# Kernel optimization log

Measured on AMD Instinct MI355X. Metric: run time of the kernel, lower is better.

Reference implementation:

```python
import jax, jax.numpy as jnp
import numpy as np

LN_EPS = 1e-5

def _layernorm(x, gamma, beta):
    mu = jnp.mean(x, axis=-1, keepdims=True)
    var = jnp.mean((x - mu) ** 2, axis=-1, keepdims=True)
    return (x - mu) / jnp.sqrt(var + LN_EPS) * gamma + beta

def setup_inputs() -> dict:
    key = jax.random.key(0)
    ks = jax.random.split(key, 12)
    B, S, D, V, H = 2, 2048, 1024, 32000, 16
    d_ff = 4 * D
    inp = {}
    inp["V"] = jax.random.randint(ks[0], (B, S), 0, V, dtype=jnp.int64)
    inp["num_heads"] = H
    sc = 0.02
    inp["emb"] = jax.random.normal(ks[1], (V, D), dtype=jnp.float32) * sc
    inp["w_o"] = jax.random.normal(ks[2], (D, D), dtype=jnp.float32) * sc
    inp["w1"] = jax.random.normal(ks[3], (D, d_ff), dtype=jnp.float32) * sc
    inp["b1"] = jnp.zeros((d_ff,), dtype=jnp.float32)
    inp["w2"] = jax.random.normal(ks[4], (d_ff, D), dtype=jnp.float32) * sc
    inp["b2"] = jnp.zeros((D,), dtype=jnp.float32)
    inp["gamma1"] = jnp.ones((D,), dtype=jnp.float32)
    inp["beta1"] = jnp.zeros((D,), dtype=jnp.float32)
    inp["gamma2"] = jnp.ones((D,), dtype=jnp.float32)
    inp["beta2"] = jnp.zeros((D,), dtype=jnp.float32)
    return inp

def reference(V, num_heads, emb, w_o, w1, b1, w2, b2, gamma1, beta1, gamma2, beta2):
    # Embedding lookup: [B, S, D]
    x = emb[V]
    B, S, D = x.shape
    hd = D // num_heads
    # NOTE: the original forward never applies w_q/w_k/w_v -- q=k=v=embedding,
    # split per head along the feature dim.
    qh = x.reshape(B, S, num_heads, hd)
    scores = jnp.einsum("bqhd,bkhd->bhqk", qh, qh) / jnp.sqrt(jnp.float32(hd))
    attn = jax.nn.softmax(scores, axis=-1)
    ctx = jnp.einsum("bhqk,bkhd->bqhd", attn, qh).reshape(B, S, D)
    attn_out = ctx @ w_o
    x1 = _layernorm(x + attn_out, gamma1, beta1)
    ff = jax.nn.relu(x1 @ w1 + b1) @ w2 + b2
    return _layernorm(x1 + ff, gamma2, beta2)
```

## Files before the change

kernel.cpp:

```cpp
#include <hip/hip_runtime.h>
#include <hip/hip_bf16.h>

#define B_  2
#define S_  2048
#define D_  1024
#define H_  16
#define HD_ 64
#define DFF 4096
#define NT  (B_ * S_)

typedef __bf16 bf16;
typedef __bf16 bf16x8 __attribute__((ext_vector_type(8)));
typedef __bf16 bf16x4 __attribute__((ext_vector_type(4)));
typedef __bf16 bf16x2 __attribute__((ext_vector_type(2)));
typedef float  f32x4  __attribute__((ext_vector_type(4)));
typedef float  f32x16 __attribute__((ext_vector_type(16)));
typedef int    i32x2  __attribute__((ext_vector_type(2)));

typedef const __attribute__((address_space(1))) unsigned int GLB_U32;
typedef __attribute__((address_space(3))) unsigned int AS3_U32;

__device__ __forceinline__ void gload16(const void* g, void* l) {
    __builtin_amdgcn_global_load_lds((GLB_U32*)g, (AS3_U32*)l, 16, 0, 0);
}

#define MFMA32(A, B, C) __builtin_amdgcn_mfma_f32_32x32x16_bf16(A, B, C, 0, 0, 0)
#define MFMA16(A, B, C) __builtin_amdgcn_mfma_f32_16x16x32_bf16(A, B, C, 0, 0, 0)

__device__ __forceinline__ unsigned pk2(float a, float b) {
    union { bf16x2 v; unsigned u; } t;
    t.v[0] = (bf16)a; t.v[1] = (bf16)b;
    return t.u;
}

#define ATT_SCL 0.18033688011112042f

#define PREP_EMB  (B_ * (S_ / 32) * (D_ / 32))
#define PREP_WO   ((D_ / 32) * (D_ / 32))
#define PREP_W1   ((D_ / 32) * (DFF / 32))
#define PREP_W2   ((DFF / 32) * (D_ / 32))
#define PREP_TOT  (PREP_EMB + PREP_WO + PREP_W1 + PREP_W2)

__device__ __forceinline__ void transcvt_tile(const float* src, bf16* dst,
                                              int R, int C, int tile,
                                              float* tf, int tx, int ty) {
    int tiles_c = C >> 5;
    int r0 = (tile / tiles_c) << 5;
    int c0 = (tile % tiles_c) << 5;
#pragma unroll
    for (int i = 0; i < 4; i++)
        tf[(ty + i * 8) * 33 + tx] = src[(size_t)(r0 + ty + i * 8) * C + c0 + tx];
    __syncthreads();
#pragma unroll
    for (int i = 0; i < 4; i++)
        dst[(size_t)(c0 + ty + i * 8) * R + r0 + tx] = (bf16)tf[tx * 33 + ty + i * 8];
}

__global__ __launch_bounds__(256)
void k_prep(const int* __restrict__ V, const float* __restrict__ emb,
            bf16* __restrict__ xb, bf16* __restrict__ xT,
            const float* __restrict__ w_o, bf16* __restrict__ wobT,
            const float* __restrict__ w1, bf16* __restrict__ w1T,
            const float* __restrict__ w2, bf16* __restrict__ w2T) {
    __shared__ float tf[32 * 33];
    int bidx = blockIdx.x;
    int tx = threadIdx.x & 31, ty = threadIdx.x >> 5;

    if (bidx < PREP_EMB) {
        bf16* tb = (bf16*)tf;
        const int tiles_d = D_ / 32;
        int b   = bidx / ((S_ / 32) * tiles_d);
        int rem = bidx % ((S_ / 32) * tiles_d);
        int ts = rem / tiles_d, td = rem % tiles_d;
        int s0 = ts * 32, d0 = td * 32;
        bf16* xbb = xb + (size_t)b * S_ * D_;
        bf16* dst = xT + (size_t)b * D_ * S_;
#pragma unroll
        for (int i = 0; i < 4; i++) {
            int srow = s0 + ty + i * 8;
            int vid = V[b * S_ + srow];
            bf16 val = (bf16)emb[(size_t)vid * D_ + d0 + tx];
            xbb[(size_t)srow * D_ + d0 + tx] = val;
            tb[(ty + i * 8) * 34 + tx] = val;
        }
        __syncthreads();
#pragma unroll
        for (int i = 0; i < 4; i++)
            dst[(size_t)(d0 + ty + i * 8) * S_ + s0 + tx] = tb[tx * 34 + ty + i * 8];
    } else if (bidx < PREP_EMB + PREP_WO) {
        transcvt_tile(w_o, wobT, D_, D_, bidx - PREP_EMB, tf, tx, ty);
    } else if (bidx < PREP_EMB + PREP_WO + PREP_W1) {
        transcvt_tile(w1, w1T, D_, DFF, bidx - PREP_EMB - PREP_WO, tf, tx, ty);
    } else {
        transcvt_tile(w2, w2T, DFF, D_, bidx - PREP_EMB - PREP_WO - PREP_W1, tf, tx, ty);
    }
}

__global__ __launch_bounds__(256)
void k_attn(const bf16* __restrict__ xb, const bf16* __restrict__ xT,
            bf16* __restrict__ ctxb) {
    __shared__ alignas(16) bf16 Kt[3][64][64];
    __shared__ alignas(16) bf16 Vt[3][64][64];

    int bh = blockIdx.x >> 4;
    int qt = blockIdx.x & 15;
    int b = bh >> 4, h = bh & 15;
    int tid = threadIdx.x;
    int w = tid >> 6, lane = tid & 63;
    int l31 = lane & 31, hi = lane >> 5;

    const bf16* xq = xb + (size_t)b * S_ * D_ + h * HD_;
    const bf16* vT = xT + ((size_t)b * D_ + h * HD_) * S_;

    int q0 = qt * 128 + w * 32;

    bf16x8 qf[4];
#pragma unroll
    for (int c = 0; c < 4; c++) {
        qf[c] = *(const bf16x8*)(xq + (size_t)(q0 + l31) * D_ + c * 16 + hi * 8);
#pragma unroll
        for (int i = 0; i < 8; i++)
            qf[c][i] = (bf16)((float)qf[c][i] * ATT_SCL);
    }

    bf16x8 onesf;
#pragma unroll
    for (int i = 0; i < 8; i++) onesf[i] = (bf16)1.0f;

    int srow = tid >> 3;
    int sbyx = ((tid & 7) << 4) ^ ((srow & 7) << 4);

    const char* kg = (const char*)(xq + (size_t)srow * D_) + sbyx;
    const char* vg = (const char*)(vT + (size_t)srow * S_) + sbyx;

    char* kdA = (char*)&Kt[0][0][0] + tid * 16;
    char* kdB = (char*)&Kt[1][0][0] + tid * 16;
    char* kdC = (char*)&Kt[2][0][0] + tid * 16;
    char* vdA = (char*)&Vt[0][0][0] + tid * 16;
    char* vdB = (char*)&Vt[1][0][0] + tid * 16;
    char* vdC = (char*)&Vt[2][0][0] + tid * 16;

    const int KSTR = 64 * D_ * 2;
    const int VSTR = 64 * 2;
    const int NTILES = S_ / 64;

    auto stage = [&](char* kd, char* vd) {
        gload16(kg, kd); gload16(kg + 32 * D_ * 2, kd + 4096);
        gload16(vg, vd); gload16(vg + 32 * S_ * 2, vd + 4096);
        kg += KSTR; vg += VSTR;
    };

    stage(kdA, vdA);
    stage(kdB, vdB);

    int rsw = (l31 & 7) << 4;
    const char* KrA = (const char*)&Kt[0][0][0] + l31 * 128;
    const char* KrB = (const char*)&Kt[1][0][0] + l31 * 128;
    const char* KrC = (const char*)&Kt[2][0][0] + l31 * 128;
    const char* VrA = (const char*)&Vt[0][0][0] + l31 * 128;
    const char* VrB = (const char*)&Vt[1][0][0] + l31 * 128;
    const char* VrC = (const char*)&Vt[2][0][0] + l31 * 128;

    f32x16 o0 = {}, o1 = {}, ol = {};

    for (int kt = 0; kt < NTILES; kt++) {
        if (kt == NTILES - 1) asm volatile("s_waitcnt vmcnt(0)" ::: "memory");
        else                  asm volatile("s_waitcnt vmcnt(4)" ::: "memory");
        __builtin_amdgcn_s_barrier();
        __builtin_amdgcn_sched_barrier(0);
        if (kt + 2 < NTILES) stage(kdC, vdC);

        const char* Kb = KrA;
        const char* Vb = VrA;

        f32x16 sa0 = {}, sa1 = {};
        {
            bf16x8 kf0[4], kf1[4];
#pragma unroll
            for (int c = 0; c < 4; c++) {
                int by = (c * 32 + hi * 16) ^ rsw;
                kf0[c] = *(const bf16x8*)(Kb + by);
                kf1[c] = *(const bf16x8*)(Kb + 32 * 128 + by);
            }
            __builtin_amdgcn_s_setprio(1);
#pragma unroll
            for (int c = 0; c < 4; c++) sa0 = MFMA32(kf0[c], qf[c], sa0);
#pragma unroll
            for (int c = 0; c < 4; c++) sa1 = MFMA32(kf1[c], qf[c], sa1);
            __builtin_amdgcn_s_setprio(0);
        }

        float p0[16], p1[16];
#pragma unroll
        for (int i = 0; i < 16; i++) p0[i] = exp2f(sa0[i]);
#pragma unroll
        for (int i = 0; i < 16; i++) p1[i] = exp2f(sa1[i]);

        union { unsigned u[4]; bf16x8 v; } pfA0, pfA1, pfB0, pfB1;
        {
            unsigned a0 = pk2(p0[0],  p0[1]),  a1 = pk2(p0[2],  p0[3]);
            unsigned a2 = pk2(p0[4],  p0[5]),  a3 = pk2(p0[6],  p0[7]);
            unsigned a4 = pk2(p0[8],  p0[9]),  a5 = pk2(p0[10], p0[11]);
            unsigned a6 = pk2(p0[12], p0[13]), a7 = pk2(p0[14], p0[15]);
            i32x2 r;
            r = __builtin_amdgcn_permlane32_swap((int)a0, (int)a2, false, false);
            pfA0.u[0] = r[0]; pfA0.u[2] = r[1];
            r = __builtin_amdgcn_permlane32_swap((int)a1, (int)a3, false, false);
            pfA0.u[1] = r[0]; pfA0.u[3] = r[1];
            r = __builtin_amdgcn_permlane32_swap((int)a4, (int)a6, false, false);
            pfA1.u[0] = r[0]; pfA1.u[2] = r[1];
            r = __builtin_amdgcn_permlane32_swap((int)a5, (int)a7, false, false);
            pfA1.u[1] = r[0]; pfA1.u[3] = r[1];
        }
        {
            unsigned a0 = pk2(p1[0],  p1[1]),  a1 = pk2(p1[2],  p1[3]);
            unsigned a2 = pk2(p1[4],  p1[5]),  a3 = pk2(p1[6],  p1[7]);
            unsigned a4 = pk2(p1[8],  p1[9]),  a5 = pk2(p1[10], p1[11]);
            unsigned a6 = pk2(p1[12], p1[13]), a7 = pk2(p1[14], p1[15]);
            i32x2 r;
            r = __builtin_amdgcn_permlane32_swap((int)a0, (int)a2, false, false);
            pfB0.u[0] = r[0]; pfB0.u[2] = r[1];
            r = __builtin_amdgcn_permlane32_swap((int)a1, (int)a3, false, false);
            pfB0.u[1] = r[0]; pfB0.u[3] = r[1];
            r = __builtin_amdgcn_permlane32_swap((int)a4, (int)a6, false, false);
            pfB1.u[0] = r[0]; pfB1.u[2] = r[1];
            r = __builtin_amdgcn_permlane32_swap((int)a5, (int)a7, false, false);
            pfB1.u[1] = r[0]; pfB1.u[3] = r[1];
        }

        {
            bf16x8 v0, v1, v2, v3;
            v0 = *(const bf16x8*)(Vb + ((0  + hi * 16) ^ rsw));
            v1 = *(const bf16x8*)(Vb + ((32 + hi * 16) ^ rsw));
            v2 = *(const bf16x8*)(Vb + ((64 + hi * 16) ^ rsw));
            v3 = *(const bf16x8*)(Vb + ((96 + hi * 16) ^ rsw));
            __builtin_amdgcn_s_setprio(1);
            o0 = MFMA32(v0, pfA0.v, o0);
            o0 = MFMA32(v1, pfA1.v, o0);
            o0 = MFMA32(v2, pfB0.v, o0);
            o0 = MFMA32(v3, pfB1.v, o0);
            ol = MFMA32(onesf, pfA0.v, ol);
            ol = MFMA32(onesf, pfA1.v, ol);
            __builtin_amdgcn_s_setprio(0);
            v0 = *(const bf16x8*)(Vb + 32 * 128 + ((0  + hi * 16) ^ rsw));
            v1 = *(const bf16x8*)(Vb + 32 * 128 + ((32 + hi * 16) ^ rsw));
            v2 = *(const bf16x8*)(Vb + 32 * 128 + ((64 + hi * 16) ^ rsw));
            v3 = *(const bf16x8*)(Vb + 32 * 128 + ((96 + hi * 16) ^ rsw));
            __builtin_amdgcn_s_setprio(1);
            o1 = MFMA32(v0, pfA0.v, o1);
            o1 = MFMA32(v1, pfA1.v, o1);
            o1 = MFMA32(v2, pfB0.v, o1);
            o1 = MFMA32(v3, pfB1.v, o1);
            ol = MFMA32(onesf, pfB0.v, ol);
            ol = MFMA32(onesf, pfB1.v, ol);
            __builtin_amdgcn_s_setprio(0);
        }

        const char* tk = KrA; KrA = KrB; KrB = KrC; KrC = tk;
        const char* tv = VrA; VrA = VrB; VrB = VrC; VrC = tv;
        char* tk2 = kdA; kdA = kdB; kdB = kdC; kdC = tk2;
        char* tv2 = vdA; vdA = vdB; vdB = vdC; vdC = tv2;
    }

    float rinv = 1.0f / ol[0];
    int q = q0 + l31;
    bf16* crow = ctxb + ((size_t)b * S_ + q) * D_ + h * HD_;
#pragma unroll
    for (int g = 0; g < 4; g++) {
        bf16x4 ov;
#pragma unroll
        for (int j = 0; j < 4; j++) ov[j] = (bf16)(o0[4 * g + j] * rinv);
        *(bf16x4*)(crow + 8 * g + 4 * hi) = ov;
    }
#pragma unroll
    for (int g = 0; g < 4; g++) {
        bf16x4 ov;
#pragma unroll
        for (int j = 0; j < 4; j++) ov[j] = (bf16)(o1[4 * g + j] * rinv);
        *(bf16x4*)(crow + 32 + 8 * g + 4 * hi) = ov;
    }
}

template <int BIAS, int RELU, int OUT_MODE>
__global__ __launch_bounds__(512)
void k_gemm256(const bf16* __restrict__ A, const bf16* __restrict__ Bt,
               const float* __restrict__ bias,
               float* __restrict__ outf, bf16* __restrict__ outb,
               int M, int N, int K) {
    __shared__ alignas(16) bf16 As[2][256][64];
    __shared__ alignas(16) bf16 Bs[2][256][64];

    int ntn = N >> 8;
    int m0 = (int)(blockIdx.x / ntn) << 8;
    int n0 = (int)(blockIdx.x % ntn) << 8;
    int tid = threadIdx.x;
    int lane = tid & 63, w = tid >> 6;
    int wm = w >> 2, wn = w & 3;
    int l15 = lane & 15, lhi = lane >> 4;
    int NK = K >> 6;

    int r0 = tid >> 3;
    int sbyx = ((tid & 7) << 4) ^ ((r0 & 7) << 4);
    const char* ag = (const char*)(A  + (size_t)(m0 + r0) * K) + sbyx;
    const char* bg = (const char*)(Bt + (size_t)(n0 + r0) * K) + sbyx;
    const size_t r64 = (size_t)64 * K * 2;

    auto stA = [&](int ob, size_t ko, int half) {
        char* d = (char*)&As[ob][0][0] + half * 16384 + tid * 16;
        gload16(ag + ko + (size_t)(2 * half) * r64, d);
        gload16(ag + ko + (size_t)(2 * half + 1) * r64, d + 8192);
    };
    auto stB = [&](int ob, size_t ko, int half) {
        char* d = (char*)&Bs[ob][0][0] + half * 16384 + tid * 16;
        gload16(bg + ko + (size_t)(2 * half) * r64, d);
        gload16(bg + ko + (size_t)(2 * half + 1) * r64, d + 8192);
    };

    stA(0, 0, 0); stA(0, 0, 1); stB(0, 0, 0); stB(0, 0, 1);

    f32x4 acc[8][4] = {};
    int rsw = (l15 & 7) << 4;
    int aro = (wm * 128 + l15) * 128;
    int bro = (wn * 64 + l15) * 128;

    for (int t = 0; t < NK; t++) {
        int buf = t & 1, ob = buf ^ 1;
        size_t ko = (size_t)(t + 1) * 128;
        const char* aB = (const char*)&As[buf][0][0] + aro;
        const char* bB = (const char*)&Bs[buf][0][0] + bro;
        bf16x8 af[4][2], bfr[4][2];

        if (t + 1 < NK) {
            stA(ob, ko, 0); stA(ob, ko, 1);
            asm volatile("s_waitcnt vmcnt(4)" ::: "memory");
        } else {
            asm volatile("s_waitcnt vmcnt(0)" ::: "memory");
        }
        __builtin_amdgcn_s_barrier();
        __builtin_amdgcn_sched_barrier(0);
#pragma unroll
        for (int mi = 0; mi < 4; mi++) {
            af[mi][0] = *(const bf16x8*)(aB + mi * 2048 + ((lhi * 16) ^ rsw));
            af[mi][1] = *(const bf16x8*)(aB + mi * 2048 + ((64 + lhi * 16) ^ rsw));
        }
#pragma unroll
        for (int ni = 0; ni < 2; ni++) {
            bfr[ni][0] = *(const bf16x8*)(bB + ni * 2048 + ((lhi * 16) ^ rsw));
            bfr[ni][1] = *(const bf16x8*)(bB + ni * 2048 + ((64 + lhi * 16) ^ rsw));
        }
        __builtin_amdgcn_s_setprio(1);
#pragma unroll
        for (int mi = 0; mi < 4; mi++)
#pragma unroll
            for (int ni = 0; ni < 2; ni++) {
                acc[mi][ni] = MFMA16(af[mi][0], bfr[ni][0], acc[mi][ni]);
                acc[mi][ni] = MFMA16(af[mi][1], bfr[ni][1], acc[mi][ni]);
            }
        __builtin_amdgcn_s_setprio(0);
        __builtin_amdgcn_s_barrier();

#pragma unroll
        for (int ni = 2; ni < 4; ni++) {
            bfr[ni][0] = *(const bf16x8*)(bB + ni * 2048 + ((lhi * 16) ^ rsw));
            bfr[ni][1] = *(const bf16x8*)(bB + ni * 2048 + ((64 + lhi * 16) ^ rsw));
        }
        if (t + 1 < NK) { stB(ob, ko, 0); stB(ob, ko, 1); }
        __builtin_amdgcn_s_barrier();
        __builtin_amdgcn_s_setprio(1);
#pragma unroll
        for (int mi = 0; mi < 4; mi++)
#pragma unroll
            for (int ni = 2; ni < 4; ni++) {
                acc[mi][ni] = MFMA16(af[mi][0], bfr[ni][0], acc[mi][ni]);
                acc[mi][ni] = MFMA16(af[mi][1], bfr[ni][1], acc[mi][ni]);
            }
        __builtin_amdgcn_s_setprio(0);
        __builtin_amdgcn_s_barrier();

#pragma unroll
        for (int mi = 0; mi < 4; mi++) {
            af[mi][0] = *(const bf16x8*)(aB + (4 + mi) * 2048 + ((lhi * 16) ^ rsw));
            af[mi][1] = *(const bf16x8*)(aB + (4 + mi) * 2048 + ((64 + lhi * 16) ^ rsw));
        }
        __builtin_amdgcn_s_barrier();
        __builtin_amdgcn_s_setprio(1);
#pragma unroll
        for (int mi = 0; mi < 4; mi++)
#pragma unroll
            for (int ni = 0; ni < 2; ni++) {
                acc[4 + mi][ni] = MFMA16(af[mi][0], bfr[ni][0], acc[4 + mi][ni]);
                acc[4 + mi][ni] = MFMA16(af[mi][1], bfr[ni][1], acc[4 + mi][ni]);
            }
        __builtin_amdgcn_s_setprio(0);
        __builtin_amdgcn_s_barrier();

        __builtin_amdgcn_s_barrier();
        __builtin_amdgcn_s_setprio(1);
#pragma unroll
        for (int mi = 0; mi < 4; mi++)
#pragma unroll
            for (int ni = 2; ni < 4; ni++) {
                acc[4 + mi][ni] = MFMA16(af[mi][0], bfr[ni][0], acc[4 + mi][ni]);
                acc[4 + mi][ni] = MFMA16(af[mi][1], bfr[ni][1], acc[4 + mi][ni]);
            }
        __builtin_amdgcn_s_setprio(0);
        __builtin_amdgcn_s_barrier();
    }

#pragma unroll
    for (int mi = 0; mi < 8; mi++) {
        int grow = m0 + wm * 128 + mi * 16 + lhi * 4;
#pragma unroll
        for (int ni = 0; ni < 4; ni++) {
            int gcol = n0 + wn * 64 + ni * 16 + l15;
            float bv = BIAS ? bias[gcol] : 0.f;
#pragma unroll
            for (int r = 0; r < 4; r++) {
                float v = acc[mi][ni][r] + bv;
                if (RELU) v = fmaxf(v, 0.f);
                size_t idx = (size_t)(grow + r) * N + gcol;
                if (OUT_MODE & 1) outf[idx] = v;
                if (OUT_MODE & 2) outb[idx] = (bf16)v;
            }
        }
    }
}

template <int BIAS, int RELU, int OUT_MODE, int SPLITK>
__global__ __launch_bounds__(512)
void k_g2(const bf16* __restrict__ A, const bf16* __restrict__ Bt,
          const float* __restrict__ bias,
          float* __restrict__ outf, bf16* __restrict__ outb,
          int M, int N, int K) {
    __shared__ alignas(16) bf16 As[2][256][64];
    __shared__ alignas(16) bf16 Bs[2][128][64];

    int ntn = N >> 7;
    int m0 = (int)(blockIdx.x / ntn) << 8;
    int n0 = (int)(blockIdx.x % ntn) << 7;
    int tid = threadIdx.x;
    int lane = tid & 63, w = tid >> 6;
    int wm = w >> 1, wn = w & 1;
    int l15 = lane & 15, lhi = lane >> 4;

    int Ks = K / SPLITK;
    int NK = Ks >> 6;
    size_t kbase = (size_t)blockIdx.y * Ks;
    float* outp = outf + (size_t)blockIdx.y * M * N;

    int srow = tid >> 3;
    int sbyx = ((tid & 7) << 4) ^ ((srow & 7) << 4);
    const char* ag = (const char*)(A  + (size_t)(m0 + srow) * K + kbase) + sbyx;
    const char* bg = (const char*)(Bt + (size_t)(n0 + srow) * K + kbase) + sbyx;
    const size_t r64 = (size_t)64 * K * 2;

    auto stA = [&](int ob, size_t ko) {
        char* d = (char*)&As[ob][0][0] + tid * 16;
        gload16(ag + ko, d);
        gload16(ag + ko + r64, d + 8192);
        gload16(ag + ko + 2 * r64, d + 16384);
        gload16(ag + ko + 3 * r64, d + 24576);
    };
    auto stB = [&](int ob, size_t ko) {
        char* d = (char*)&Bs[ob][0][0] + tid * 16;
        gload16(bg + ko, d);
        gload16(bg + ko + r64, d + 8192);
    };

    stA(0, 0); stB(0, 0);

    f32x4 acc[4][4] = {};
    int rsw = (l15 & 7) << 4;
    int aro = (wm * 64 + l15) * 128;
    int bro = (wn * 64 + l15) * 128;

    for (int t = 0; t < NK; t++) {
        int buf = t & 1, ob = buf ^ 1;
        size_t ko = (size_t)(t + 1) * 128;
        const char* aB = (const char*)&As[buf][0][0] + aro;
        const char* bB = (const char*)&Bs[buf][0][0] + bro;
        bf16x8 af[4][2], bn[4][2];

        if (t + 1 < NK) {
            stA(ob, ko);
            asm volatile("s_waitcnt vmcnt(4)" ::: "memory");
        } else {
            asm volatile("s_waitcnt vmcnt(0)" ::: "memory");
        }
        __builtin_amdgcn_s_barrier();
        __builtin_amdgcn_sched_barrier(0);
#pragma unroll
        for (int mi = 0; mi < 4; mi++)
            af[mi][0] = *(const bf16x8*)(aB + mi * 2048 + ((lhi * 16) ^ rsw));
#pragma unroll
        for (int ni = 0; ni < 4; ni++)
            bn[ni][0] = *(const bf16x8*)(bB + ni * 2048 + ((lhi * 16) ^ rsw));
        __builtin_amdgcn_s_setprio(1);
#pragma unroll
        for (int mi = 0; mi < 4; mi++)
#pragma unroll
            for (int ni = 0; ni < 4; ni++)
                acc[mi][ni] = MFMA16(af[mi][0], bn[ni][0], acc[mi][ni]);
        __builtin_amdgcn_s_setprio(0);
        __builtin_amdgcn_s_barrier();

#pragma unroll
        for (int mi = 0; mi < 4; mi++)
            af[mi][1] = *(const bf16x8*)(aB + mi * 2048 + ((64 + lhi * 16) ^ rsw));
#pragma unroll
        for (int ni = 0; ni < 4; ni++)
            bn[ni][1] = *(const bf16x8*)(bB + ni * 2048 + ((64 + lhi * 16) ^ rsw));
        if (t + 1 < NK) stB(ob, ko);
        __builtin_amdgcn_s_barrier();
        __builtin_amdgcn_s_setprio(1);
#pragma unroll
        for (int mi = 0; mi < 4; mi++)
#pragma unroll
            for (int ni = 0; ni < 4; ni++)
                acc[mi][ni] = MFMA16(af[mi][1], bn[ni][1], acc[mi][ni]);
        __builtin_amdgcn_s_setprio(0);
        __builtin_amdgcn_s_barrier();
    }

#pragma unroll
    for (int mi = 0; mi < 4; mi++) {
        int grow = m0 + wm * 64 + mi * 16 + lhi * 4;
#pragma unroll
        for (int ni = 0; ni < 4; ni++) {
            int gcol = n0 + wn * 64 + ni * 16 + l15;
            float bv = BIAS ? bias[gcol] : 0.f;
#pragma unroll
            for (int r = 0; r < 4; r++) {
                float v = acc[mi][ni][r] + bv;
                if (RELU) v = fmaxf(v, 0.f);
                size_t idx = (size_t)(grow + r) * N + gcol;
                if (OUT_MODE & 1) outp[idx] = v;
                if (OUT_MODE & 2) outb[idx] = (bf16)v;
            }
        }
    }
}

__global__ __launch_bounds__(256)
void k_ln1(const float* __restrict__ pA, const bf16* __restrict__ resb,
           const float* __restrict__ gamma, const float* __restrict__ beta,
           bf16* __restrict__ x1b) {
    const float* pB = pA + (size_t)NT * D_;
    int row = blockIdx.x, tid = threadIdx.x;
    size_t base = (size_t)row * D_ + tid * 4;
    float4 a = *(const float4*)(pA + base);
    float4 c = *(const float4*)(pB + base);
    bf16x4 rb = *(const bf16x4*)(resb + base);
    float4 v;
    v.x = a.x + c.x + (float)rb[0];
    v.y = a.y + c.y + (float)rb[1];
    v.z = a.z + c.z + (float)rb[2];
    v.w = a.w + c.w + (float)rb[3];
    float s  = v.x + v.y + v.z + v.w;
    float sq = v.x * v.x + v.y * v.y + v.z * v.z + v.w * v.w;
#pragma unroll
    for (int m = 1; m < 64; m <<= 1) {
        s  += __shfl_xor(s, m, 64);
        sq += __shfl_xor(sq, m, 64);
    }
    __shared__ float ss[4], ssq[4];
    int w = tid >> 6;
    if ((tid & 63) == 0) { ss[w] = s; ssq[w] = sq; }
    __syncthreads();
    s  = ss[0] + ss[1] + ss[2] + ss[3];
    sq = ssq[0] + ssq[1] + ssq[2] + ssq[3];
    float mu  = s * (1.f / D_);
    float var = sq * (1.f / D_) - mu * mu;
    float rstd = rsqrtf(var + 1e-5f);
    float4 g  = *(const float4*)(gamma + tid * 4);
    float4 bt = *(const float4*)(beta + tid * 4);
    bf16x4 ob;
    ob[0] = (bf16)((v.x - mu) * rstd * g.x + bt.x);
    ob[1] = (bf16)((v.y - mu) * rstd * g.y + bt.y);
    ob[2] = (bf16)((v.z - mu) * rstd * g.z + bt.z);
    ob[3] = (bf16)((v.w - mu) * rstd * g.w + bt.w);
    *(bf16x4*)(x1b + base) = ob;
}

__global__ __launch_bounds__(256)
void k_ln2(const float* __restrict__ pA, const float* __restrict__ bias,
           const bf16* __restrict__ resb,
           const float* __restrict__ gamma, const float* __restrict__ beta,
           float* __restrict__ out) {
    const float* pB = pA + (size_t)NT * D_;
    int row = blockIdx.x, tid = threadIdx.x;
    size_t base = (size_t)row * D_ + tid * 4;
    float4 a = *(const float4*)(pA + base);
    float4 c = *(const float4*)(pB + base);
    bf16x4 rb = *(const bf16x4*)(resb + base);
    float4 bb = *(const float4*)(bias + tid * 4);
    float4 v;
    v.x = a.x + c.x + (float)rb[0] + bb.x;
    v.y = a.y + c.y + (float)rb[1] + bb.y;
    v.z = a.z + c.z + (float)rb[2] + bb.z;
    v.w = a.w + c.w + (float)rb[3] + bb.w;
    float s  = v.x + v.y + v.z + v.w;
    float sq = v.x * v.x + v.y * v.y + v.z * v.z + v.w * v.w;
#pragma unroll
    for (int m = 1; m < 64; m <<= 1) {
        s  += __shfl_xor(s, m, 64);
        sq += __shfl_xor(sq, m, 64);
    }
    __shared__ float ss[4], ssq[4];
    int w = tid >> 6;
    if ((tid & 63) == 0) { ss[w] = s; ssq[w] = sq; }
    __syncthreads();
    s  = ss[0] + ss[1] + ss[2] + ss[3];
    sq = ssq[0] + ssq[1] + ssq[2] + ssq[3];
    float mu  = s * (1.f / D_);
    float var = sq * (1.f / D_) - mu * mu;
    float rstd = rsqrtf(var + 1e-5f);
    float4 g  = *(const float4*)(gamma + tid * 4);
    float4 bt = *(const float4*)(beta + tid * 4);
    float4 o;
    o.x = (v.x - mu) * rstd * g.x + bt.x;
    o.y = (v.y - mu) * rstd * g.y + bt.y;
    o.z = (v.z - mu) * rstd * g.z + bt.z;
    o.w = (v.w - mu) * rstd * g.w + bt.w;
    *(float4*)(out + base) = o;
}

extern "C" void kernel_launch(void* const* d_in, const int* in_sizes, int n_in,
                              void* d_out, int out_size, void* d_ws, size_t ws_size,
                              hipStream_t stream) {
    const int*   Vi  = (const int*)d_in[0];
    const float* emb = (const float*)d_in[2];
    const float* w_o = (const float*)d_in[3];
    const float* w1  = (const float*)d_in[4];
    const float* b1  = (const float*)d_in[5];
    const float* w2  = (const float*)d_in[6];
    const float* b2  = (const float*)d_in[7];
    const float* g1  = (const float*)d_in[8];
    const float* be1 = (const float*)d_in[9];
    const float* g2  = (const float*)d_in[10];
    const float* be2 = (const float*)d_in[11];
    float* out = (float*)d_out;

    char* ws = (char*)d_ws;
    size_t off = 0;
    auto alloc = [&](size_t bytes) -> void* {
        void* p = ws + off;
        off += (bytes + 255) & ~(size_t)255;
        return p;
    };
    bf16*  xb   = (bf16*)alloc((size_t)NT * D_ * 2);
    bf16*  xT   = (bf16*)alloc((size_t)NT * D_ * 2);
    bf16*  wobT = (bf16*)alloc((size_t)D_ * D_ * 2);
    bf16*  w1T  = (bf16*)alloc((size_t)DFF * D_ * 2);
    bf16*  w2T  = (bf16*)alloc((size_t)D_ * DFF * 2);
    bf16*  ctxb = (bf16*)alloc((size_t)NT * D_ * 2);
    bf16*  x1b  = (bf16*)alloc((size_t)NT * D_ * 2);
    bf16*  h1   = (bf16*)alloc((size_t)NT * DFF * 2);
    float* RB   = (float*)alloc((size_t)2 * NT * D_ * 4);
    float* g1p  = RB;
    float* g3p  = RB;

    k_prep<<<PREP_TOT, 256, 0, stream>>>(Vi, emb, xb, xT, w_o, wobT, w1, w1T, w2, w2T);

    k_attn<<<32 * (S_ / 128), 256, 0, stream>>>(xb, xT, ctxb);

    k_g2<0, 0, 1, 2><<<dim3((NT / 256) * (D_ / 128), 2), 512, 0, stream>>>(
        ctxb, wobT, nullptr, g1p, nullptr, NT, D_, D_);
    k_ln1<<<NT, 256, 0, stream>>>(g1p, xb, g1, be1, x1b);

    k_gemm256<1, 1, 2><<<(NT / 256) * (DFF / 256), 512, 0, stream>>>(
        x1b, w1T, b1, nullptr, h1, NT, DFF, D_);

    k_g2<0, 0, 1, 2><<<dim3((NT / 256) * (D_ / 128), 2), 512, 0, stream>>>(
        h1, w2T, nullptr, g3p, nullptr, NT, D_, DFF);
    k_ln2<<<NT, 256, 0, stream>>>(g3p, b2, x1b, g2, be2, out);
}
```

Measured before the change: 208.4 us.

## Store split-K partials as bf16 and use split-K 256-tile GEMM for FFN2

```diff
diff --git a/kernel.cpp b/kernel.cpp
--- a/kernel.cpp
+++ b/kernel.cpp
@@ -281,7 +281,7 @@
     }
 }
 
-template <int BIAS, int RELU, int OUT_MODE>
+template <int BIAS, int RELU, int OUT_MODE, int SPLITK>
 __global__ __launch_bounds__(512)
 void k_gemm256(const bf16* __restrict__ A, const bf16* __restrict__ Bt,
                const float* __restrict__ bias,
@@ -297,12 +297,17 @@
     int lane = tid & 63, w = tid >> 6;
     int wm = w >> 2, wn = w & 3;
     int l15 = lane & 15, lhi = lane >> 4;
-    int NK = K >> 6;
+
+    int Ks = K / SPLITK;
+    int NK = Ks >> 6;
+    size_t kbase = (size_t)blockIdx.y * Ks;
+    float* outpf = outf ? outf + (size_t)blockIdx.y * M * N : nullptr;
+    bf16*  outpb = outb ? outb + (size_t)blockIdx.y * M * N : nullptr;
 
     int r0 = tid >> 3;
     int sbyx = ((tid & 7) << 4) ^ ((r0 & 7) << 4);
-    const char* ag = (const char*)(A  + (size_t)(m0 + r0) * K) + sbyx;
-    const char* bg = (const char*)(Bt + (size_t)(n0 + r0) * K) + sbyx;
+    const char* ag = (const char*)(A  + (size_t)(m0 + r0) * K + kbase) + sbyx;
+    const char* bg = (const char*)(Bt + (size_t)(n0 + r0) * K + kbase) + sbyx;
     const size_t r64 = (size_t)64 * K * 2;
 
     auto stA = [&](int ob, size_t ko, int half) {
@@ -419,8 +424,8 @@
                 float v = acc[mi][ni][r] + bv;
                 if (RELU) v = fmaxf(v, 0.f);
                 size_t idx = (size_t)(grow + r) * N + gcol;
-                if (OUT_MODE & 1) outf[idx] = v;
-                if (OUT_MODE & 2) outb[idx] = (bf16)v;
+                if (OUT_MODE & 1) outpf[idx] = v;
+                if (OUT_MODE & 2) outpb[idx] = (bf16)v;
             }
         }
     }
@@ -446,7 +451,8 @@
     int Ks = K / SPLITK;
     int NK = Ks >> 6;
     size_t kbase = (size_t)blockIdx.y * Ks;
-    float* outp = outf + (size_t)blockIdx.y * M * N;
+    float* outpf = outf ? outf + (size_t)blockIdx.y * M * N : nullptr;
+    bf16*  outpb = outb ? outb + (size_t)blockIdx.y * M * N : nullptr;
 
     int srow = tid >> 3;
     int sbyx = ((tid & 7) << 4) ^ ((srow & 7) << 4);
@@ -483,7 +489,7 @@
 
         if (t + 1 < NK) {
             stA(ob, ko);
-            asm volatile("s_waitcnt vmcnt(4)" ::: "memory");
+            asm volatile("s_waitcnt vmcnt(2)" ::: "memory");
         } else {
             asm volatile("s_waitcnt vmcnt(0)" ::: "memory");
         }
@@ -534,28 +540,27 @@
                 float v = acc[mi][ni][r] + bv;
                 if (RELU) v = fmaxf(v, 0.f);
                 size_t idx = (size_t)(grow + r) * N + gcol;
-                if (OUT_MODE & 1) outp[idx] = v;
-                if (OUT_MODE & 2) outb[idx] = (bf16)v;
+                if (OUT_MODE & 1) outpf[idx] = v;
+                if (OUT_MODE & 2) outpb[idx] = (bf16)v;
             }
         }
     }
 }
 
 __global__ __launch_bounds__(256)
-void k_ln1(const float* __restrict__ pA, const bf16* __restrict__ resb,
+void k_ln1(const bf16* __restrict__ p, const bf16* __restrict__ resb,
            const float* __restrict__ gamma, const float* __restrict__ beta,
            bf16* __restrict__ x1b) {
-    const float* pB = pA + (size_t)NT * D_;
     int row = blockIdx.x, tid = threadIdx.x;
     size_t base = (size_t)row * D_ + tid * 4;
-    float4 a = *(const float4*)(pA + base);
-    float4 c = *(const float4*)(pB + base);
+    bf16x4 a = *(const bf16x4*)(p + base);
+    bf16x4 c = *(const bf16x4*)(p + (size_t)NT * D_ + base);
     bf16x4 rb = *(const bf16x4*)(resb + base);
     float4 v;
-    v.x = a.x + c.x + (float)rb[0];
-    v.y = a.y + c.y + (float)rb[1];
-    v.z = a.z + c.z + (float)rb[2];
-    v.w = a.w + c.w + (float)rb[3];
+    v.x = (float)a[0] + (float)c[0] + (float)rb[0];
+    v.y = (float)a[1] + (float)c[1] + (float)rb[1];
+    v.z = (float)a[2] + (float)c[2] + (float)rb[2];
+    v.w = (float)a[3] + (float)c[3] + (float)rb[3];
     float s  = v.x + v.y + v.z + v.w;
     float sq = v.x * v.x + v.y * v.y + v.z * v.z + v.w * v.w;
 #pragma unroll
@@ -583,22 +588,23 @@
 }
 
 __global__ __launch_bounds__(256)
-void k_ln2(const float* __restrict__ pA, const float* __restrict__ bias,
+void k_ln2(const bf16* __restrict__ p, const float* __restrict__ bias,
            const bf16* __restrict__ resb,
            const float* __restrict__ gamma, const float* __restrict__ beta,
            float* __restrict__ out) {
-    const float* pB = pA + (size_t)NT * D_;
     int row = blockIdx.x, tid = threadIdx.x;
     size_t base = (size_t)row * D_ + tid * 4;
-    float4 a = *(const float4*)(pA + base);
-    float4 c = *(const float4*)(pB + base);
+    bf16x4 s0 = *(const bf16x4*)(p + base);
+    bf16x4 s1 = *(const bf16x4*)(p + (size_t)NT * D_ + base);
+    bf16x4 s2 = *(const bf16x4*)(p + (size_t)2 * NT * D_ + base);
+    bf16x4 s3 = *(const bf16x4*)(p + (size_t)3 * NT * D_ + base);
     bf16x4 rb = *(const bf16x4*)(resb + base);
     float4 bb = *(const float4*)(bias + tid * 4);
     float4 v;
-    v.x = a.x + c.x + (float)rb[0] + bb.x;
-    v.y = a.y + c.y + (float)rb[1] + bb.y;
-    v.z = a.z + c.z + (float)rb[2] + bb.z;
-    v.w = a.w + c.w + (float)rb[3] + bb.w;
+    v.x = ((float)s0[0] + (float)s1[0]) + ((float)s2[0] + (float)s3[0]) + (float)rb[0] + bb.x;
+    v.y = ((float)s0[1] + (float)s1[1]) + ((float)s2[1] + (float)s3[1]) + (float)rb[1] + bb.y;
+    v.z = ((float)s0[2] + (float)s1[2]) + ((float)s2[2] + (float)s3[2]) + (float)rb[2] + bb.z;
+    v.w = ((float)s0[3] + (float)s1[3]) + ((float)s2[3] + (float)s3[3]) + (float)rb[3] + bb.w;
     float s  = v.x + v.y + v.z + v.w;
     float sq = v.x * v.x + v.y * v.y + v.z * v.z + v.w * v.w;
 #pragma unroll
@@ -656,22 +662,22 @@
     bf16*  ctxb = (bf16*)alloc((size_t)NT * D_ * 2);
     bf16*  x1b  = (bf16*)alloc((size_t)NT * D_ * 2);
     bf16*  h1   = (bf16*)alloc((size_t)NT * DFF * 2);
-    float* RB   = (float*)alloc((size_t)2 * NT * D_ * 4);
-    float* g1p  = RB;
-    float* g3p  = RB;
+    bf16*  RB   = (bf16*)alloc((size_t)4 * NT * D_ * 2);
+    bf16*  g1pb = RB;
+    bf16*  g3pb = RB;
 
     k_prep<<<PREP_TOT, 256, 0, stream>>>(Vi, emb, xb, xT, w_o, wobT, w1, w1T, w2, w2T);
 
     k_attn<<<32 * (S_ / 128), 256, 0, stream>>>(xb, xT, ctxb);
 
-    k_g2<0, 0, 1, 2><<<dim3((NT / 256) * (D_ / 128), 2), 512, 0, stream>>>(
-        ctxb, wobT, nullptr, g1p, nullptr, NT, D_, D_);
-    k_ln1<<<NT, 256, 0, stream>>>(g1p, xb, g1, be1, x1b);
-
-    k_gemm256<1, 1, 2><<<(NT / 256) * (DFF / 256), 512, 0, stream>>>(
+    k_g2<0, 0, 2, 2><<<dim3((NT / 256) * (D_ / 128), 2), 512, 0, stream>>>(
+        ctxb, wobT, nullptr, nullptr, g1pb, NT, D_, D_);
+    k_ln1<<<NT, 256, 0, stream>>>(g1pb, xb, g1, be1, x1b);
+
+    k_gemm256<1, 1, 2, 1><<<(NT / 256) * (DFF / 256), 512, 0, stream>>>(
         x1b, w1T, b1, nullptr, h1, NT, DFF, D_);
 
-    k_g2<0, 0, 1, 2><<<dim3((NT / 256) * (D_ / 128), 2), 512, 0, stream>>>(
-        h1, w2T, nullptr, g3p, nullptr, NT, D_, DFF);
-    k_ln2<<<NT, 256, 0, stream>>>(g3p, b2, x1b, g2, be2, out);
-}
+    k_gemm256<0, 0, 2, 4><<<dim3((NT / 256) * (D_ / 256), 4), 512, 0, stream>>>(
+        h1, w2T, nullptr, nullptr, g3pb, NT, D_, DFF);
+    k_ln2<<<NT, 256, 0, stream>>>(g3pb, b2, x1b, g2, be2, out);
+}
```

After: 199.0 us (median of 2 runs). 1.05x faster.
